# Performance work log

Measured on AMD Instinct MI355X. Metric: run time of the kernel, lower is better.

The kernel has to match this reference:

```python
import jax, jax.numpy as jnp
import numpy as np

N_NODES = 100000
N_EDGES = 1600000
DIM = 128
BN_EPS = 1e-5


def setup_inputs() -> dict:
    key = jax.random.key(0)
    k1, k2, k3, k4 = jax.random.split(key, 4)
    scale = 1.0 / np.sqrt(DIM)
    return {
        "x": jax.random.normal(k1, (N_NODES, DIM), dtype=jnp.float32),
        "edge_index": jax.random.randint(k2, (2, N_EDGES), 0, N_NODES, dtype=jnp.int64),
        "W_l": jax.random.normal(k3, (DIM, DIM), dtype=jnp.float32) * scale,
        "b_l": jnp.zeros((DIM,), dtype=jnp.float32),
        "W_r": jax.random.normal(k4, (DIM, DIM), dtype=jnp.float32) * scale,
        "gamma": jnp.ones((DIM,), dtype=jnp.float32),
        "beta": jnp.zeros((DIM,), dtype=jnp.float32),
    }


def reference(x, edge_index, W_l, b_l, W_r, gamma, beta):
    n = x.shape[0]
    src, dst = edge_index[0], edge_index[1]
    # SAGEConv mean aggregation: gather source features, scatter-sum to dst, divide by degree
    agg = jax.ops.segment_sum(x[src], dst, num_segments=n)          # [N, d_in]
    deg = jax.ops.segment_sum(jnp.ones_like(src, dtype=x.dtype), dst, num_segments=n)
    mean = agg / jnp.maximum(deg, 1.0)[:, None]
    # lin_l(mean) + lin_r(x)  (bias lives in lin_l, PyG default)
    h = mean @ W_l + b_l + x @ W_r                                   # [N, d_out]
    # act -> BatchNorm1d (training mode, batch stats) -> dropout(p=0, identity)
    h = jax.nn.relu(h)
    mu = jnp.mean(h, axis=0)
    var = jnp.mean(jnp.square(h - mu), axis=0)                       # biased var, as torch BN
    h = (h - mu) * jax.lax.rsqrt(var + BN_EPS) * gamma + beta
    # residual
    return x + h
```

## Files before the change

kernel.cpp:

```cpp
#include <hip/hip_runtime.h>

#define DIM 128
#define BN_EPS 1e-5f
#define NB 32
#define NBK_MAX 512

typedef __attribute__((ext_vector_type(8))) short bf16x8;
typedef __attribute__((ext_vector_type(4))) float f32x4;

union B8 { uint4 u; bf16x8 s; };

__device__ __forceinline__ ushort f2bf(float f) {
    unsigned u = __float_as_uint(f);
    u += 0x7fffu + ((u >> 16) & 1u);
    return (ushort)(u >> 16);
}

__global__ void k_prep(const float4* __restrict__ x4, const float* __restrict__ Wl,
                       const float* __restrict__ Wr, const unsigned* __restrict__ eiu,
                       int* __restrict__ bcnt, uint2* __restrict__ xf8,
                       uint4* __restrict__ wpack, int nn, int ne, int PB, int WB) {
    __shared__ int nz;
    __shared__ int lh[NBK_MAX];
    int b = blockIdx.x;
    const int tid = threadIdx.x;

    if (b < PB) {
        const int t = b * 256 + tid;
        const int n8 = nn * DIM / 8;
        if (t < n8) {
            const float4 a = x4[2 * t], c = x4[2 * t + 1];
            int u0 = __builtin_amdgcn_cvt_pk_fp8_f32(a.x, a.y, 0, false);
            u0 = __builtin_amdgcn_cvt_pk_fp8_f32(a.z, a.w, u0, true);
            int u1 = __builtin_amdgcn_cvt_pk_fp8_f32(c.x, c.y, 0, false);
            u1 = __builtin_amdgcn_cvt_pk_fp8_f32(c.z, c.w, u1, true);
            xf8[t] = make_uint2((unsigned)u0, (unsigned)u1);
        }
        return;
    }
    b -= PB;
    if (b < WB) {
        const int t = b * 256 + tid;
        const int lane = t & 63, kk = (t >> 6) & 3, nt = (t >> 8) & 7, mat = t >> 11;
        const float* W = mat ? Wr : Wl;
        const int k0 = kk * 32 + (lane >> 4) * 8;
        const int n = nt * 16 + (lane & 15);
        ushort e[8];
#pragma unroll
        for (int j = 0; j < 8; ++j) e[j] = f2bf(W[(size_t)(k0 + j) * DIM + n]);
        uint4 o;
        o.x = ((unsigned)e[1] << 16) | e[0];
        o.y = ((unsigned)e[3] << 16) | e[2];
        o.z = ((unsigned)e[5] << 16) | e[4];
        o.w = ((unsigned)e[7] << 16) | e[6];
        wpack[t] = o;
        return;
    }
    b -= WB;
    const int nbk = (nn + 255) >> 8;
    for (int i = tid; i < nbk; i += 256) lh[i] = 0;
    if (tid == 0) nz = 0;
    __syncthreads();
    const int e0 = b * 4096;
    {
        int es = e0 + tid * 16;
        if (es >= ne) es = ne - 1;
        if (eiu[2 * (size_t)es + 1] != 0) atomicOr(&nz, 1);
    }
    __syncthreads();
    const int is64 = (nz == 0);
    for (int j = 0; j < 16; ++j) {
        const int e = e0 + j * 256 + tid;
        if (e < ne) {
            int dst;
            if (is64) dst = (int)((const long long*)eiu)[(size_t)ne + e];
            else      dst = ((const int*)eiu)[(size_t)ne + e];
            atomicAdd(&lh[dst >> 8], 1);
        }
    }
    __syncthreads();
    for (int i = tid; i < nbk; i += 256)
        if (lh[i]) atomicAdd(&bcnt[i], lh[i]);
}

__global__ __launch_bounds__(512) void k_scanb(const int* __restrict__ bcnt,
                                               int* __restrict__ bbase,
                                               int* __restrict__ cursor2, int nn, int ne) {
    __shared__ int sd[512];
    const int nbk = (nn + 255) >> 8;
    const int tid = threadIdx.x;
    const int v = (tid < nbk) ? bcnt[tid] : 0;
    sd[tid] = v;
    __syncthreads();
    for (int ofs = 1; ofs < 512; ofs <<= 1) {
        const int t = (tid >= ofs) ? sd[tid - ofs] : 0;
        __syncthreads();
        sd[tid] += t;
        __syncthreads();
    }
    if (tid < nbk) {
        const int ex = sd[tid] - v;
        bbase[tid] = ex;
        cursor2[tid] = ex;
    }
    if (tid == 0) bbase[nbk] = ne;
}

__global__ __launch_bounds__(256) void k_passA(const unsigned* __restrict__ eiu,
                                               int* __restrict__ cursor2,
                                               unsigned* __restrict__ pairbuf,
                                               int nn, int ne) {
    __shared__ int lh[NBK_MAX];
    __shared__ int gb[NBK_MAX];
    __shared__ int nz;
    const int nbk = (nn + 255) >> 8;
    const int tid = threadIdx.x;
    const int e0 = blockIdx.x * 4096;
    for (int i = tid; i < nbk; i += 256) lh[i] = 0;
    if (tid == 0) nz = 0;
    __syncthreads();
    {
        int es = e0 + tid * 16;
        if (es >= ne) es = ne - 1;
        if (eiu[2 * (size_t)es + 1] != 0) atomicOr(&nz, 1);
    }
    __syncthreads();
    const int is64 = (nz == 0);
    unsigned pay[16];
    int bkrank[16];
#pragma unroll
    for (int j = 0; j < 16; ++j) {
        const int e = e0 + j * 256 + tid;
        bkrank[j] = -1;
        if (e < ne) {
            int src, dst;
            if (is64) {
                const long long* p = (const long long*)eiu;
                src = (int)p[e];
                dst = (int)p[(size_t)ne + e];
            } else {
                const int* p = (const int*)eiu;
                src = p[e];
                dst = p[(size_t)ne + e];
            }
            const int bk = dst >> 8;
            const int rank = atomicAdd(&lh[bk], 1);
            bkrank[j] = (bk << 16) | rank;
            pay[j] = ((unsigned)(dst & 255) << 24) | (unsigned)src;
        }
    }
    __syncthreads();
    for (int i = tid; i < nbk; i += 256) {
        const int c = lh[i];
        gb[i] = c ? atomicAdd(&cursor2[i], c) : 0;
    }
    __syncthreads();
#pragma unroll
    for (int j = 0; j < 16; ++j) {
        if (bkrank[j] >= 0) {
            const int bk = bkrank[j] >> 16, rank = bkrank[j] & 0xFFFF;
            pairbuf[gb[bk] + rank] = pay[j];
        }
    }
}

__global__ __launch_bounds__(256) void k_passB(const unsigned* __restrict__ pairbuf,
                                               const int* __restrict__ bbase,
                                               int* __restrict__ off, int* __restrict__ cnt,
                                               int* __restrict__ srcbuf, int nn) {
    __shared__ int cl[256];
    __shared__ int sd[256];
    __shared__ int cur[256];
    const int tid = threadIdx.x;
    const int b = blockIdx.x;
    const int node0 = b << 8;
    const int e0 = bbase[b], e1 = bbase[b + 1];
    cl[tid] = 0;
    __syncthreads();
    for (int e = e0 + tid; e < e1; e += 256)
        atomicAdd(&cl[pairbuf[e] >> 24], 1);
    __syncthreads();
    const int v = cl[tid];
    sd[tid] = v;
    __syncthreads();
    for (int ofs = 1; ofs < 256; ofs <<= 1) {
        const int t = (tid >= ofs) ? sd[tid - ofs] : 0;
        __syncthreads();
        sd[tid] += t;
        __syncthreads();
    }
    const int ex = sd[tid] - v;
    cur[tid] = ex;
    const int node = node0 + tid;
    if (node < nn) {
        off[node] = e0 + ex;
        cnt[node] = v;
    }
    __syncthreads();
    for (int e = e0 + tid; e < e1; e += 256) {
        const unsigned p = pairbuf[e];
        const int pos = atomicAdd(&cur[p >> 24], 1);
        srcbuf[e0 + pos] = (int)(p & 0xFFFFFFu);
    }
}

__global__ __launch_bounds__(512, 4) void k_gemm(
    const float4* __restrict__ x4g, const uint2* __restrict__ xf8,
    const uint4* __restrict__ wpack, const float* __restrict__ bl,
    const int* __restrict__ off, const int* __restrict__ cnt,
    const int* __restrict__ srcbuf,
    ushort* __restrict__ hout, float* __restrict__ ssum, float* __restrict__ ssq,
    int nn)
{
    __shared__ uint4 mean4[NB * 16];
    __shared__ uint4 xls4[NB * 16];
    __shared__ float red_sum[2][DIM];
    __shared__ float red_sq[2][DIM];

    const int tid = threadIdx.x;
    const int lane = tid & 63;
    const int w = tid >> 6;
    const int base = blockIdx.x * NB;
    const int g = lane >> 4;
    const int q = lane & 15;

    {
        const int ln = w * 4 + g;
        const int node = base + ln;
        float acc[8];
#pragma unroll
        for (int j = 0; j < 8; ++j) acc[j] = 0.f;
        uint4 xp = make_uint4(0, 0, 0, 0);

        if (node < nn) {
            const float4 xa = x4g[(size_t)node * 32 + 2 * q];
            const float4 xb = x4g[(size_t)node * 32 + 2 * q + 1];
            xp.x = ((unsigned)f2bf(xa.y) << 16) | f2bf(xa.x);
            xp.y = ((unsigned)f2bf(xa.w) << 16) | f2bf(xa.z);
            xp.z = ((unsigned)f2bf(xb.y) << 16) | f2bf(xb.x);
            xp.w = ((unsigned)f2bf(xb.w) << 16) | f2bf(xb.z);

            const int o = off[node];
            const int c = cnt[node];
            int e = 0;
            for (; e + 4 <= c; e += 4) {
                const int s0 = srcbuf[o + e + 0];
                const int s1 = srcbuf[o + e + 1];
                const int s2 = srcbuf[o + e + 2];
                const int s3 = srcbuf[o + e + 3];
                const uint2 v0 = xf8[(unsigned)(s0 * 16 + q)];
                const uint2 v1 = xf8[(unsigned)(s1 * 16 + q)];
                const uint2 v2 = xf8[(unsigned)(s2 * 16 + q)];
                const uint2 v3 = xf8[(unsigned)(s3 * 16 + q)];
#pragma unroll
                for (int k = 0; k < 4; ++k) {
                    const uint2 v = (k == 0) ? v0 : (k == 1) ? v1 : (k == 2) ? v2 : v3;
                    auto p0 = __builtin_amdgcn_cvt_pk_f32_fp8(v.x, false);
                    auto p1 = __builtin_amdgcn_cvt_pk_f32_fp8(v.x, true);
                    auto p2 = __builtin_amdgcn_cvt_pk_f32_fp8(v.y, false);
                    auto p3 = __builtin_amdgcn_cvt_pk_f32_fp8(v.y, true);
                    acc[0] += p0[0]; acc[1] += p0[1]; acc[2] += p1[0]; acc[3] += p1[1];
                    acc[4] += p2[0]; acc[5] += p2[1]; acc[6] += p3[0]; acc[7] += p3[1];
                }
            }
            for (; e < c; ++e) {
                const int s = srcbuf[o + e];
                const uint2 v = xf8[(unsigned)(s * 16 + q)];
                auto p0 = __builtin_amdgcn_cvt_pk_f32_fp8(v.x, false);
                auto p1 = __builtin_amdgcn_cvt_pk_f32_fp8(v.x, true);
                auto p2 = __builtin_amdgcn_cvt_pk_f32_fp8(v.y, false);
                auto p3 = __builtin_amdgcn_cvt_pk_f32_fp8(v.y, true);
                acc[0] += p0[0]; acc[1] += p0[1]; acc[2] += p1[0]; acc[3] += p1[1];
                acc[4] += p2[0]; acc[5] += p2[1]; acc[6] += p3[0]; acc[7] += p3[1];
            }
            const float r = 1.0f / fmaxf((float)c, 1.0f);
#pragma unroll
            for (int j = 0; j < 8; ++j) acc[j] *= r;
        }

        uint4 mp;
        mp.x = ((unsigned)f2bf(acc[1]) << 16) | f2bf(acc[0]);
        mp.y = ((unsigned)f2bf(acc[3]) << 16) | f2bf(acc[2]);
        mp.z = ((unsigned)f2bf(acc[5]) << 16) | f2bf(acc[4]);
        mp.w = ((unsigned)f2bf(acc[7]) << 16) | f2bf(acc[6]);
        const int slot = q ^ (ln & 15);
        mean4[ln * 16 + slot] = mp;
        xls4[ln * 16 + slot] = xp;
    }
    __syncthreads();

    const int m = w & 1;
    const int nh = w >> 1;
    const int row16 = lane & 15;
    const int kgrp = lane >> 4;
    const int ln2 = m * 16 + row16;

    bf16x8 am[4], ax[4];
#pragma unroll
    for (int kk = 0; kk < 4; ++kk) {
        const int unit = (kk * 4 + kgrp) ^ row16;
        B8 va, vb;
        va.u = mean4[ln2 * 16 + unit];
        vb.u = xls4[ln2 * 16 + unit];
        am[kk] = va.s;
        ax[kk] = vb.s;
    }

    f32x4 acc[2];
#pragma unroll
    for (int j = 0; j < 2; ++j) {
        const float bv = bl[(nh * 2 + j) * 16 + row16];
        acc[j] = (f32x4){bv, bv, bv, bv};
    }

#pragma unroll
    for (int j = 0; j < 2; ++j) {
        const int nt = nh * 2 + j;
        const uint4* pl = wpack + (size_t)(nt * 4) * 64 + lane;
        const uint4* pr = wpack + (size_t)((8 + nt) * 4) * 64 + lane;
        B8 wl[4], wr[4];
#pragma unroll
        for (int kk = 0; kk < 4; ++kk) {
            wl[kk].u = pl[kk * 64];
            wr[kk].u = pr[kk * 64];
        }
#pragma unroll
        for (int kk = 0; kk < 4; ++kk)
            acc[j] = __builtin_amdgcn_mfma_f32_16x16x32_bf16(am[kk], wl[kk].s, acc[j], 0, 0, 0);
#pragma unroll
        for (int kk = 0; kk < 4; ++kk)
            acc[j] = __builtin_amdgcn_mfma_f32_16x16x32_bf16(ax[kk], wr[kk].s, acc[j], 0, 0, 0);
    }

#pragma unroll
    for (int j = 0; j < 2; ++j) {
        const int feat = (nh * 2 + j) * 16 + row16;
        float s = 0.f, sq = 0.f;
#pragma unroll
        for (int r = 0; r < 4; ++r) {
            const int node = base + m * 16 + kgrp * 4 + r;
            const float v = fmaxf(acc[j][r], 0.0f);
            if (node < nn) {
                hout[(size_t)node * DIM + feat] = f2bf(v);
                s += v;
                sq += v * v;
            }
        }
        s += __shfl_xor(s, 16);
        s += __shfl_xor(s, 32);
        sq += __shfl_xor(sq, 16);
        sq += __shfl_xor(sq, 32);
        if (lane < 16) {
            red_sum[m][feat] = s;
            red_sq[m][feat] = sq;
        }
    }
    __syncthreads();
    if (tid < DIM) {
        atomicAdd(&ssum[tid], red_sum[0][tid] + red_sum[1][tid]);
        atomicAdd(&ssq[tid], red_sq[0][tid] + red_sq[1][tid]);
    }
}

__global__ __launch_bounds__(512) void k_finalize(
    const float4* __restrict__ x4, const uint4* __restrict__ h4,
    const float* __restrict__ ssum, const float* __restrict__ ssq,
    const float* __restrict__ gamma, const float* __restrict__ beta,
    float4* __restrict__ out4, int nn)
{
    const float invN = 1.0f / (float)nn;
    const int tid = threadIdx.x;
    const int node = blockIdx.x * 32 + (tid >> 4);
    const int q = tid & 15;
    if (node >= nn) return;
    const uint4 hv = h4[(size_t)node * 16 + q];
    const float4 xa = x4[(size_t)node * 32 + 2 * q];
    const float4 xb = x4[(size_t)node * 32 + 2 * q + 1];
    const float4 s4a = ((const float4*)ssum)[2 * q], s4b = ((const float4*)ssum)[2 * q + 1];
    const float4 q4a = ((const float4*)ssq)[2 * q], q4b = ((const float4*)ssq)[2 * q + 1];
    const float4 g4a = ((const float4*)gamma)[2 * q], g4b = ((const float4*)gamma)[2 * q + 1];
    const float4 b4a = ((const float4*)beta)[2 * q], b4b = ((const float4*)beta)[2 * q + 1];
    float h[8];
    h[0] = __uint_as_float(hv.x << 16);
    h[1] = __uint_as_float(hv.x & 0xffff0000u);
    h[2] = __uint_as_float(hv.y << 16);
    h[3] = __uint_as_float(hv.y & 0xffff0000u);
    h[4] = __uint_as_float(hv.z << 16);
    h[5] = __uint_as_float(hv.z & 0xffff0000u);
    h[6] = __uint_as_float(hv.w << 16);
    h[7] = __uint_as_float(hv.w & 0xffff0000u);
    float4 oa, ob;
    {
        const float mu = s4a.x * invN, rs = rsqrtf(q4a.x * invN - mu * mu + BN_EPS);
        oa.x = xa.x + (h[0] - mu) * rs * g4a.x + b4a.x;
    }
    {
        const float mu = s4a.y * invN, rs = rsqrtf(q4a.y * invN - mu * mu + BN_EPS);
        oa.y = xa.y + (h[1] - mu) * rs * g4a.y + b4a.y;
    }
    {
        const float mu = s4a.z * invN, rs = rsqrtf(q4a.z * invN - mu * mu + BN_EPS);
        oa.z = xa.z + (h[2] - mu) * rs * g4a.z + b4a.z;
    }
    {
        const float mu = s4a.w * invN, rs = rsqrtf(q4a.w * invN - mu * mu + BN_EPS);
        oa.w = xa.w + (h[3] - mu) * rs * g4a.w + b4a.w;
    }
    {
        const float mu = s4b.x * invN, rs = rsqrtf(q4b.x * invN - mu * mu + BN_EPS);
        ob.x = xb.x + (h[4] - mu) * rs * g4b.x + b4b.x;
    }
    {
        const float mu = s4b.y * invN, rs = rsqrtf(q4b.y * invN - mu * mu + BN_EPS);
        ob.y = xb.y + (h[5] - mu) * rs * g4b.y + b4b.y;
    }
    {
        const float mu = s4b.z * invN, rs = rsqrtf(q4b.z * invN - mu * mu + BN_EPS);
        ob.z = xb.z + (h[6] - mu) * rs * g4b.z + b4b.z;
    }
    {
        const float mu = s4b.w * invN, rs = rsqrtf(q4b.w * invN - mu * mu + BN_EPS);
        ob.w = xb.w + (h[7] - mu) * rs * g4b.w + b4b.w;
    }
    out4[(size_t)node * 32 + 2 * q] = oa;
    out4[(size_t)node * 32 + 2 * q + 1] = ob;
}

extern "C" void kernel_launch(void* const* d_in, const int* in_sizes, int n_in,
                              void* d_out, int out_size, void* d_ws, size_t ws_size,
                              hipStream_t stream) {
    const float* x     = (const float*)d_in[0];
    const void*  ei    = d_in[1];
    const float* Wl    = (const float*)d_in[2];
    const float* bl    = (const float*)d_in[3];
    const float* Wr    = (const float*)d_in[4];
    const float* gamma = (const float*)d_in[5];
    const float* beta  = (const float*)d_in[6];
    float* out = (float*)d_out;

    const int nn = in_sizes[0] / DIM;
    const int ne = in_sizes[1] / 2;
    const int nbk = (nn + 255) >> 8;

    int* ws = (int*)d_ws;
    int*   bcnt    = ws;
    float* ssum    = (float*)(ws + 512);
    float* ssq     = (float*)(ws + 640);
    int*   bbase   = ws + 768;
    int*   cursor2 = ws + 1280;
    int*   cnt     = ws + 1792;
    int*   off     = cnt + nn;
    size_t pos = 1792 + 2 * (size_t)nn;
    pos = (pos + 3) & ~(size_t)3;
    uint4* wpack  = (uint4*)(ws + pos);
    int*   srcbuf = (int*)(wpack + 4096);
    size_t p2 = (size_t)(srcbuf + ne - ws);
    p2 = (p2 + 3) & ~(size_t)3;
    uint2* xf8 = (uint2*)(ws + p2);
    unsigned* pairbuf = (unsigned*)(xf8 + (size_t)nn * 16);
    ushort*   hbuf    = (ushort*)pairbuf;

    hipMemsetAsync(d_ws, 0, 768 * sizeof(int), stream);

    const int PB = (nn * DIM / 8 + 255) / 256;
    const int WB = 16;
    const int HB = (ne + 4095) / 4096;
    k_prep<<<PB + WB + HB, 256, 0, stream>>>((const float4*)x, Wl, Wr,
                                             (const unsigned*)ei, bcnt, xf8, wpack,
                                             nn, ne, PB, WB);
    k_scanb<<<1, 512, 0, stream>>>(bcnt, bbase, cursor2, nn, ne);
    k_passA<<<(ne + 4095) / 4096, 256, 0, stream>>>((const unsigned*)ei, cursor2,
                                                    pairbuf, nn, ne);
    k_passB<<<nbk, 256, 0, stream>>>(pairbuf, bbase, off, cnt, srcbuf, nn);
    const int ntile = (nn + NB - 1) / NB;
    k_gemm<<<ntile, 512, 0, stream>>>((const float4*)x, xf8, wpack, bl, off, cnt,
                                      srcbuf, hbuf, ssum, ssq, nn);
    k_finalize<<<ntile, 512, 0, stream>>>((const float4*)x, (const uint4*)hbuf,
                                          ssum, ssq, gamma, beta, (float4*)out, nn);
}
```

Before: 187.3 us.

## Split FP8 feature table into four planes and gather edges in parallel per plane

The FP8 copy of x is stored as four 32-feature planes instead of one 128-byte row per node. In the gather, each 16-lane group now processes four edges at once, with each edge reading a 32-byte chunk of one plane, and loops over the four planes. Partial sums are combined with cross-lane shuffles before the mean is written to shared memory. The aim is to give more independent gathers per lane and a plane-sized working set that may stay in cache better, at the cost of re-reading edge indices for every plane plus extra shuffles and loop overhead.

```diff
diff --git a/kernel.cpp b/kernel.cpp
--- a/kernel.cpp
+++ b/kernel.cpp
@@ -34,7 +34,10 @@
             u0 = __builtin_amdgcn_cvt_pk_fp8_f32(a.z, a.w, u0, true);
             int u1 = __builtin_amdgcn_cvt_pk_fp8_f32(c.x, c.y, 0, false);
             u1 = __builtin_amdgcn_cvt_pk_fp8_f32(c.z, c.w, u1, true);
-            xf8[t] = make_uint2((unsigned)u0, (unsigned)u1);
+            const int node = t >> 4;
+            const int wd = t & 15;
+            const int p = wd >> 2, f = wd & 3;
+            xf8[((size_t)p * nn + node) * 4 + f] = make_uint2((unsigned)u0, (unsigned)u1);
         }
         return;
     }
@@ -221,17 +224,25 @@
     const int lane = tid & 63;
     const int w = tid >> 6;
     const int base = blockIdx.x * NB;
-    const int g = lane >> 4;
     const int q = lane & 15;
-
-    {
-        const int ln = w * 4 + g;
+    const int es = q >> 2;
+    const int f = q & 3;
+
+#define CVT8(v)                                                           \
+    {                                                                     \
+        auto p0 = __builtin_amdgcn_cvt_pk_f32_fp8((v).x, false);          \
+        auto p1 = __builtin_amdgcn_cvt_pk_f32_fp8((v).x, true);           \
+        auto p2 = __builtin_amdgcn_cvt_pk_f32_fp8((v).y, false);          \
+        auto p3 = __builtin_amdgcn_cvt_pk_f32_fp8((v).y, true);           \
+        acc[0] += p0[0]; acc[1] += p0[1]; acc[2] += p1[0]; acc[3] += p1[1]; \
+        acc[4] += p2[0]; acc[5] += p2[1]; acc[6] += p3[0]; acc[7] += p3[1]; \
+    }
+
+    {
+        const int ln = w * 4 + (lane >> 4);
         const int node = base + ln;
-        float acc[8];
-#pragma unroll
-        for (int j = 0; j < 8; ++j) acc[j] = 0.f;
         uint4 xp = make_uint4(0, 0, 0, 0);
-
+        int o = 0, c = 0;
         if (node < nn) {
             const float4 xa = x4g[(size_t)node * 32 + 2 * q];
             const float4 xb = x4g[(size_t)node * 32 + 2 * q + 1];
@@ -239,54 +250,57 @@
             xp.y = ((unsigned)f2bf(xa.w) << 16) | f2bf(xa.z);
             xp.z = ((unsigned)f2bf(xb.y) << 16) | f2bf(xb.x);
             xp.w = ((unsigned)f2bf(xb.w) << 16) | f2bf(xb.z);
-
-            const int o = off[node];
-            const int c = cnt[node];
-            int e = 0;
-            for (; e + 4 <= c; e += 4) {
-                const int s0 = srcbuf[o + e + 0];
-                const int s1 = srcbuf[o + e + 1];
-                const int s2 = srcbuf[o + e + 2];
-                const int s3 = srcbuf[o + e + 3];
-                const uint2 v0 = xf8[(unsigned)(s0 * 16 + q)];
-                const uint2 v1 = xf8[(unsigned)(s1 * 16 + q)];
-                const uint2 v2 = xf8[(unsigned)(s2 * 16 + q)];
-                const uint2 v3 = xf8[(unsigned)(s3 * 16 + q)];
-#pragma unroll
-                for (int k = 0; k < 4; ++k) {
-                    const uint2 v = (k == 0) ? v0 : (k == 1) ? v1 : (k == 2) ? v2 : v3;
-                    auto p0 = __builtin_amdgcn_cvt_pk_f32_fp8(v.x, false);
-                    auto p1 = __builtin_amdgcn_cvt_pk_f32_fp8(v.x, true);
-                    auto p2 = __builtin_amdgcn_cvt_pk_f32_fp8(v.y, false);
-                    auto p3 = __builtin_amdgcn_cvt_pk_f32_fp8(v.y, true);
-                    acc[0] += p0[0]; acc[1] += p0[1]; acc[2] += p1[0]; acc[3] += p1[1];
-                    acc[4] += p2[0]; acc[5] += p2[1]; acc[6] += p3[0]; acc[7] += p3[1];
+            o = off[node];
+            c = cnt[node];
+        }
+        xls4[ln * 16 + (q ^ (ln & 15))] = xp;
+        const float r = 1.0f / fmaxf((float)c, 1.0f);
+
+#pragma unroll
+        for (int p = 0; p < 4; ++p) {
+            const uint2* __restrict__ plane = xf8 + (size_t)p * nn * 4;
+            float acc[8];
+#pragma unroll
+            for (int j = 0; j < 8; ++j) acc[j] = 0.f;
+            if (node < nn) {
+                int e = 0;
+                for (; e + 8 <= c; e += 8) {
+                    const int s0 = srcbuf[o + e + es];
+                    const int s1 = srcbuf[o + e + 4 + es];
+                    const uint2 v0 = plane[(size_t)s0 * 4 + f];
+                    const uint2 v1 = plane[(size_t)s1 * 4 + f];
+                    CVT8(v0);
+                    CVT8(v1);
+                }
+                for (; e + 4 <= c; e += 4) {
+                    const int s = srcbuf[o + e + es];
+                    const uint2 v = plane[(size_t)s * 4 + f];
+                    CVT8(v);
+                }
+                const int rem = c - e;
+                if (es < rem) {
+                    const int s = srcbuf[o + e + es];
+                    const uint2 v = plane[(size_t)s * 4 + f];
+                    CVT8(v);
                 }
             }
-            for (; e < c; ++e) {
-                const int s = srcbuf[o + e];
-                const uint2 v = xf8[(unsigned)(s * 16 + q)];
-                auto p0 = __builtin_amdgcn_cvt_pk_f32_fp8(v.x, false);
-                auto p1 = __builtin_amdgcn_cvt_pk_f32_fp8(v.x, true);
-                auto p2 = __builtin_amdgcn_cvt_pk_f32_fp8(v.y, false);
-                auto p3 = __builtin_amdgcn_cvt_pk_f32_fp8(v.y, true);
-                acc[0] += p0[0]; acc[1] += p0[1]; acc[2] += p1[0]; acc[3] += p1[1];
-                acc[4] += p2[0]; acc[5] += p2[1]; acc[6] += p3[0]; acc[7] += p3[1];
+#pragma unroll
+            for (int j = 0; j < 8; ++j) {
+                acc[j] += __shfl_xor(acc[j], 4);
+                acc[j] += __shfl_xor(acc[j], 8);
+                acc[j] *= r;
             }
-            const float r = 1.0f / fmaxf((float)c, 1.0f);
-#pragma unroll
-            for (int j = 0; j < 8; ++j) acc[j] *= r;
-        }
-
-        uint4 mp;
-        mp.x = ((unsigned)f2bf(acc[1]) << 16) | f2bf(acc[0]);
-        mp.y = ((unsigned)f2bf(acc[3]) << 16) | f2bf(acc[2]);
-        mp.z = ((unsigned)f2bf(acc[5]) << 16) | f2bf(acc[4]);
-        mp.w = ((unsigned)f2bf(acc[7]) << 16) | f2bf(acc[6]);
-        const int slot = q ^ (ln & 15);
-        mean4[ln * 16 + slot] = mp;
-        xls4[ln * 16 + slot] = xp;
-    }
+            if (es == 0) {
+                uint4 mp;
+                mp.x = ((unsigned)f2bf(acc[1]) << 16) | f2bf(acc[0]);
+                mp.y = ((unsigned)f2bf(acc[3]) << 16) | f2bf(acc[2]);
+                mp.z = ((unsigned)f2bf(acc[5]) << 16) | f2bf(acc[4]);
+                mp.w = ((unsigned)f2bf(acc[7]) << 16) | f2bf(acc[6]);
+                mean4[ln * 16 + ((p * 4 + f) ^ (ln & 15))] = mp;
+            }
+        }
+    }
+#undef CVT8
     __syncthreads();
 
     const int m = w & 1;
@@ -306,11 +320,11 @@
         ax[kk] = vb.s;
     }
 
-    f32x4 acc[2];
+    f32x4 acc2[2];
 #pragma unroll
     for (int j = 0; j < 2; ++j) {
         const float bv = bl[(nh * 2 + j) * 16 + row16];
-        acc[j] = (f32x4){bv, bv, bv, bv};
+        acc2[j] = (f32x4){bv, bv, bv, bv};
     }
 
 #pragma unroll
@@ -326,10 +340,10 @@
         }
 #pragma unroll
         for (int kk = 0; kk < 4; ++kk)
-            acc[j] = __builtin_amdgcn_mfma_f32_16x16x32_bf16(am[kk], wl[kk].s, acc[j], 0, 0, 0);
+            acc2[j] = __builtin_amdgcn_mfma_f32_16x16x32_bf16(am[kk], wl[kk].s, acc2[j], 0, 0, 0);
 #pragma unroll
         for (int kk = 0; kk < 4; ++kk)
-            acc[j] = __builtin_amdgcn_mfma_f32_16x16x32_bf16(ax[kk], wr[kk].s, acc[j], 0, 0, 0);
+            acc2[j] = __builtin_amdgcn_mfma_f32_16x16x32_bf16(ax[kk], wr[kk].s, acc2[j], 0, 0, 0);
     }
 
 #pragma unroll
@@ -339,7 +353,7 @@
 #pragma unroll
         for (int r = 0; r < 4; ++r) {
             const int node = base + m * 16 + kgrp * 4 + r;
-            const float v = fmaxf(acc[j][r], 0.0f);
+            const float v = fmaxf(acc2[j][r], 0.0f);
             if (node < nn) {
                 hout[(size_t)node * DIM + feat] = f2bf(v);
                 s += v;
@@ -473,8 +487,8 @@
                                                     pairbuf, nn, ne);
     k_passB<<<nbk, 256, 0, stream>>>(pairbuf, bbase, off, cnt, srcbuf, nn);
     const int ntile = (nn + NB - 1) / NB;
-    k_gemm<<<ntile, 512, 0, stream>>>((const float4*)x, xf8, wpack, bl, off, cnt,
-                                      srcbuf, hbuf, ssum, ssq, nn);
+    k_gemm<<<ntile, 512, 0, stream>>>((const float4*)x, xf8, wpack, bl,
+                                      off, cnt, srcbuf, hbuf, ssum, ssq, nn);
     k_finalize<<<ntile, 512, 0, stream>>>((const float4*)x, (const uint4*)hbuf,
                                           ssum, ssq, gamma, beta, (float4*)out, nn);
 }
```

New measurement: 209.0 us. 11.6% more time.
